# Kernel optimization log

Measured on AMD Instinct MI355X. Metric: run time of the kernel, lower is better.

## Reference

```python
import jax, jax.numpy as jnp
import numpy as np

N, P, EA, EP = 2000, 10000, 60000, 150000
F, K, L = 128, 30, 3
CUTOFF = 4.0
NUM_Z = 119  # len(ase.data.atomic_numbers)


def cosine_cutoff(d, cutoff):
    return jnp.where(d < cutoff, 0.5 * (jnp.cos(jnp.pi * d / cutoff) + 1.0), 0.0)


def sinc_expansion(d, n, cutoff):
    # d: [E,1] -> [E,n]: sin(k*pi*d/cutoff)/d, via normalized sinc
    k = jnp.arange(1, n + 1, dtype=d.dtype)
    return jnp.sinc(d * k / cutoff) * (jnp.pi * k / cutoff)


def mlp2(x, w1, b1, w2, b2):
    return jax.nn.silu(x @ w1 + b1) @ w2 + b2


def painn_update(s, v, U, V, w1, b1, w2, b2):
    Uv = jnp.einsum('nif,fg->nig', v, U)
    Vv = jnp.einsum('nif,fg->nig', v, V)
    Vv_norm = jnp.linalg.norm(Vv, axis=1)  # [n,F]
    a = mlp2(jnp.concatenate([s, Vv_norm], axis=1), w1, b1, w2, b2)  # [n,3F]
    f = s.shape[1]
    a_ss, a_sv, a_vv = a[:, :f], a[:, f:2 * f], a[:, 2 * f:]
    inner = jnp.sum(Uv * Vv, axis=1)  # [n,F]
    return s + a_ss + a_sv * inner, v + a_vv[:, None, :] * Uv


def edge_messages(sender_s, sender_v, edge_state, edge_diff, edge_dist, src,
                  fw, fb, w1, b1, w2, b2, cutoff):
    f = sender_s.shape[1]
    unit = edge_diff / jnp.maximum(jnp.linalg.norm(edge_diff, axis=1, keepdims=True), 1e-12)
    filt = (edge_state @ fw + fb) * cosine_cutoff(edge_dist, cutoff)  # [E,3F]
    out = filt * mlp2(sender_s, w1, b1, w2, b2)[src]  # gather sender scalar features
    g_sv, g_ev, g_ss = out[:, :f], out[:, f:2 * f], out[:, 2 * f:]
    msg_v = sender_v[src] * g_sv[:, None, :] + g_ev[:, None, :] * unit[:, :, None]  # [E,3,F]
    return g_ss, msg_v


def setup_inputs():
    key = jax.random.key(0)
    def nrm(i, shape, scale=0.05):
        return jax.random.normal(jax.random.fold_in(key, i), shape, dtype=jnp.float32) * scale
    atom_xyz = jax.random.uniform(jax.random.fold_in(key, 100), (N, 3), dtype=jnp.float32) * 5.0
    probe_xyz = jax.random.uniform(jax.random.fold_in(key, 101), (P, 3), dtype=jnp.float32) * 5.0
    cell = jnp.eye(3, dtype=jnp.float32) * 5.0 + nrm(102, (3, 3), 0.01)
    nodes_Z = jax.random.randint(jax.random.fold_in(key, 103), (N,), 0, NUM_Z)
    a_src = jax.random.randint(jax.random.fold_in(key, 104), (EA,), 0, N)
    a_dst = (a_src + 1 + jax.random.randint(jax.random.fold_in(key, 105), (EA,), 0, N - 1)) % N  # no self-edges
    atom_edges = jnp.stack([a_src, a_dst], axis=1)
    p_src = jax.random.randint(jax.random.fold_in(key, 106), (EP,), 0, N)
    p_dst = jax.random.randint(jax.random.fold_in(key, 107), (EP,), 0, P)
    probe_edges = jnp.stack([p_src, p_dst], axis=1)
    return dict(
        atom_xyz=atom_xyz, probe_xyz=probe_xyz, cell=cell,
        atom_edges_disp=jnp.zeros((EA, 3), jnp.float32),
        probe_edges_disp=jnp.zeros((EP, 3), jnp.float32),
        atom_embed=nrm(0, (NUM_Z, F), 1.0),
        ai_filter_w=nrm(1, (L, K, 3 * F)), ai_filter_b=nrm(2, (L, 3 * F)),
        ai_w1=nrm(3, (L, F, F)), ai_b1=nrm(4, (L, F)),
        ai_w2=nrm(5, (L, F, 3 * F)), ai_b2=nrm(6, (L, 3 * F)),
        au_U=nrm(7, (L, F, F)), au_V=nrm(8, (L, F, F)),
        au_w1=nrm(9, (L, 2 * F, F)), au_b1=nrm(10, (L, F)),
        au_w2=nrm(11, (L, F, 3 * F)), au_b2=nrm(12, (L, 3 * F)),
        pm_filter_w=nrm(13, (L, K, 3 * F)), pm_filter_b=nrm(14, (L, 3 * F)),
        pm_w1=nrm(15, (L, F, F)), pm_b1=nrm(16, (L, F)),
        pm_w2=nrm(17, (L, F, 3 * F)), pm_b2=nrm(18, (L, 3 * F)),
        pm_gw1=nrm(19, (L, F, 2 * F)), pm_gb1=nrm(20, (L, 2 * F)),
        pm_gw2=nrm(21, (L, 2 * F, 2 * F)), pm_gb2=nrm(22, (L, 2 * F)),
        pu_U=nrm(23, (L, F, F)), pu_V=nrm(24, (L, F, F)),
        pu_w1=nrm(25, (L, 2 * F, F)), pu_b1=nrm(26, (L, F)),
        pu_w2=nrm(27, (L, F, 3 * F)), pu_b2=nrm(28, (L, 3 * F)),
        nodes_Z=nodes_Z, atom_edges=atom_edges, probe_edges=probe_edges,
    )


def reference(atom_xyz, probe_xyz, cell, atom_edges_disp, probe_edges_disp, atom_embed,
              ai_filter_w, ai_filter_b, ai_w1, ai_b1, ai_w2, ai_b2,
              au_U, au_V, au_w1, au_b1, au_w2, au_b2,
              pm_filter_w, pm_filter_b, pm_w1, pm_b1, pm_w2, pm_b2,
              pm_gw1, pm_gb1, pm_gw2, pm_gb2,
              pu_U, pu_V, pu_w1, pu_b1, pu_w2, pu_b2,
              nodes_Z, atom_edges, probe_edges):
    # ---- atom representation model ----
    a_src, a_dst = atom_edges[:, 0], atom_edges[:, 1]
    a_diff = atom_xyz[a_dst] - (atom_xyz[a_src] + atom_edges_disp @ cell)  # [EA,3]
    a_dist = jnp.linalg.norm(a_diff, axis=1, keepdims=True)  # [EA,1]
    a_state = sinc_expansion(a_dist, K, CUTOFF)  # [EA,K]

    s = atom_embed[nodes_Z]  # [N,F]
    v = jnp.zeros((s.shape[0], 3, F), dtype=s.dtype)
    s_list, v_list = [], []
    for l in range(L):
        g_ss, msg_v = edge_messages(s, v, a_state, a_diff, a_dist, a_src,
                                    ai_filter_w[l], ai_filter_b[l], ai_w1[l], ai_b1[l],
                                    ai_w2[l], ai_b2[l], CUTOFF)
        s = s + jax.ops.segment_sum(g_ss, a_dst, num_segments=N)
        v = v + jax.ops.segment_sum(msg_v, a_dst, num_segments=N)
        s, v = painn_update(s, v, au_U[l], au_V[l], au_w1[l], au_b1[l], au_w2[l], au_b2[l])
        s_list.append(s)
        v_list.append(v)

    # ---- probe message model (one-way, gated update) ----
    p_src, p_dst = probe_edges[:, 0], probe_edges[:, 1]
    p_diff = probe_xyz[p_dst] - (atom_xyz[p_src] + probe_edges_disp @ cell)  # [EP,3]
    p_dist = jnp.linalg.norm(p_diff, axis=1, keepdims=True)
    p_state = sinc_expansion(p_dist, K, CUTOFF)

    ps = jnp.zeros((P, F), dtype=s.dtype)
    pv = jnp.zeros((P, 3, F), dtype=s.dtype)
    for l in range(L):
        g_ss, msg_v = edge_messages(s_list[l], v_list[l], p_state, p_diff, p_dist, p_src,
                                    pm_filter_w[l], pm_filter_b[l], pm_w1[l], pm_b1[l],
                                    pm_w2[l], pm_b2[l], CUTOFF)
        m_s = jax.ops.segment_sum(g_ss, p_dst, num_segments=P)
        m_v = jax.ops.segment_sum(msg_v, p_dst, num_segments=P)
        gate = jax.nn.sigmoid(mlp2(m_s, pm_gw1[l], pm_gb1[l], pm_gw2[l], pm_gb2[l]))  # [P,2F]
        gs, gv = gate[:, :F], gate[:, F:]
        ps = ps * gs + (1.0 - gs) * m_s
        pv = pv * gv[:, None, :] + (1.0 - gv[:, None, :]) * m_v
        ps, pv = painn_update(ps, pv, pu_U[l], pu_V[l], pu_w1[l], pu_b1[l], pu_w2[l], pu_b2[l])
    return ps, pv
```

## Files before the change

### kernel.cpp

```cpp
#include <hip/hip_runtime.h>
#include <hip/hip_bf16.h>
#include <math.h>

#define PI_F 3.14159265358979323846f

static constexpr int F = 128;
static constexpr int KB = 30;
static constexpr int LAYERS = 3;
static constexpr float CUT = 4.0f;
static constexpr int BINS = 512;

typedef short bf16x8 __attribute__((ext_vector_type(8)));
typedef float f32x4 __attribute__((ext_vector_type(4)));
typedef unsigned short u16x8 __attribute__((ext_vector_type(8)));

__device__ __forceinline__ float bf2f(unsigned short u) {
    union { unsigned int i; float f; } c; c.i = ((unsigned int)u) << 16; return c.f;
}
__device__ __forceinline__ short f2bf(float x) {
    union { float f; unsigned int u; } c; c.f = x;
    unsigned int r = c.u + 0x7FFFu + ((c.u >> 16) & 1u);
    return (short)(r >> 16);
}

__device__ __forceinline__ float edge_dist(const float* __restrict__ sxyz,
                                           const float* __restrict__ dxyz,
                                           const float* __restrict__ disp,
                                           const float* __restrict__ cell,
                                           int s, int d, int e, float* dx) {
    const float* dp = disp + 3 * (size_t)e;
#pragma unroll
    for (int i = 0; i < 3; i++) {
        float dc = dp[0] * cell[0 * 3 + i] + dp[1] * cell[1 * 3 + i] + dp[2] * cell[2 * 3 + i];
        dx[i] = dxyz[3 * d + i] - (sxyz[3 * s + i] + dc);
    }
    return sqrtf(dx[0] * dx[0] + dx[1] * dx[1] + dx[2] * dx[2]);
}

__global__ void k_count(const int* __restrict__ edges, const float* __restrict__ sxyz,
                        const float* __restrict__ dxyz, const float* __restrict__ disp,
                        const float* __restrict__ cell, int* __restrict__ cnt, int E) {
    int i = blockIdx.x * blockDim.x + threadIdx.x;
    if (i >= E) return;
    int s = edges[2 * i], d = edges[2 * i + 1];
    float dx[3];
    float dist = edge_dist(sxyz, dxyz, disp, cell, s, d, i, dx);
    if (dist < CUT) atomicAdd(&cnt[d], 1);
}

__global__ void k_scan(const int* __restrict__ cnt, int* __restrict__ off, int n) {
    __shared__ int part[1024];
    int t = threadIdx.x;
    int chunk = (n + 1023) / 1024;
    int b = t * chunk; if (b > n) b = n;
    int e = b + chunk; if (e > n) e = n;
    int s = 0;
    for (int i = b; i < e; i++) s += cnt[i];
    part[t] = s;
    __syncthreads();
    for (int o = 1; o < 1024; o <<= 1) {
        int v = part[t];
        int add = (t >= o) ? part[t - o] : 0;
        __syncthreads();
        part[t] = v + add;
        __syncthreads();
    }
    int run = (t == 0) ? 0 : part[t - 1];
    for (int i = b; i < e; i++) { off[i] = run; run += cnt[i]; }
    if (t == 1023) off[n] = part[1023];
}

__global__ void k_scatter(const int* __restrict__ edges, const float* __restrict__ sxyz,
                          const float* __restrict__ dxyz, const float* __restrict__ disp,
                          const float* __restrict__ cell, int* __restrict__ cur,
                          int* __restrict__ eids, int E) {
    int i = blockIdx.x * blockDim.x + threadIdx.x;
    if (i >= E) return;
    int s = edges[2 * i], d = edges[2 * i + 1];
    float dx[3];
    float dist = edge_dist(sxyz, dxyz, disp, cell, s, d, i, dx);
    if (dist < CUT) {
        int pos = atomicAdd(&cur[d], 1);
        eids[pos] = i;
    }
}

__global__ void k_geom_rec(const float* __restrict__ sxyz, const float* __restrict__ dxyz,
                           const float* __restrict__ disp, const float* __restrict__ cell,
                           const int* __restrict__ edges, const int* __restrict__ eids,
                           const int* __restrict__ eoff, int ndst,
                           float4* __restrict__ erec, int* __restrict__ srcs) {
    int pos = blockIdx.x * blockDim.x + threadIdx.x;
    if (pos >= eoff[ndst]) return;
    int e = eids[pos];
    int s = edges[2 * e], d = edges[2 * e + 1];
    float dx[3];
    float dist = edge_dist(sxyz, dxyz, disp, cell, s, d, e, dx);
    float inv = 1.0f / fmaxf(dist, 1e-12f);
    float db = fminf(dist * ((float)BINS / CUT), (float)BINS - 0.0001f);
    erec[pos] = make_float4(dx[0] * inv, dx[1] * inv, dx[2] * inv, db);
    srcs[pos] = s;
}

__global__ void k_sbuild(float* __restrict__ Sp) {
    int i = blockIdx.x * blockDim.x + threadIdx.x;
    if (i > BINS) return;
    float d = (float)i * (CUT / (float)BINS);
    float cc = (d < CUT) ? 0.5f * (cosf(PI_F * d / CUT) + 1.0f) : 0.0f;
    float* row = Sp + (size_t)i * 32;
#pragma unroll
    for (int k = 0; k < KB; k++) {
        float kk = (float)(k + 1);
        float st = (d > 1e-12f) ? sinf(PI_F * d * kk / CUT) / d : PI_F * kk / CUT;
        row[k] = cc * st;
    }
    row[30] = cc;
    row[31] = 0.f;
}

__global__ void k_fwpack(const float* __restrict__ ai_fw, const float* __restrict__ ai_fb,
                         const float* __restrict__ pm_fw, const float* __restrict__ pm_fb,
                         float* __restrict__ fwp) {
    int i = blockIdx.x * blockDim.x + threadIdx.x;
    if (i >= 6 * 32 * 384) return;
    int tbl = i / (32 * 384);
    int k = (i / 384) % 32;
    int c = i % 384;
    const float* fw = (tbl < 3) ? ai_fw + (size_t)tbl * KB * 384 : pm_fw + (size_t)(tbl - 3) * KB * 384;
    const float* fb = (tbl < 3) ? ai_fb + (size_t)tbl * 384 : pm_fb + (size_t)(tbl - 3) * 384;
    float v = 0.f;
    if (k < KB) v = fw[(size_t)k * 384 + c];
    else if (k == 30) v = fb[c];
    fwp[i] = v;
}

__global__ void k_tpack(const short* __restrict__ Tbf, short* __restrict__ Tp) {
    int i = blockIdx.x * blockDim.x + threadIdx.x;
    if (i >= 6 * BINS * 128) return;
    int tbl = i / (BINS * 128);
    int rem = i % (BINS * 128);
    int bin = rem >> 7, lane = rem & 127;
    const short* a = Tbf + ((size_t)tbl * (BINS + 1) + bin) * 512 + lane * 4;
    const short* b = a + 512;
    short* o = Tp + ((size_t)tbl * BINS + bin) * 1024 + lane * 8;
    o[0] = a[0]; o[1] = a[1]; o[2] = a[2]; o[3] = 0;
    o[4] = b[0]; o[5] = b[1]; o[6] = b[2]; o[7] = 0;
}

struct CvtArgs {
    const float* src[14];
    int dstoff[14];
    int Kk[14];
    int Nn[14];
};
__global__ __launch_bounds__(256) void k_cvtw(CvtArgs a, short* __restrict__ dst) {
    int arr = blockIdx.y, l = blockIdx.z;
    int K = a.Kk[arr], N = a.Nn[arr];
    int tilesx = N / 32, tilesy = K / 32;
    int tile = blockIdx.x;
    if (tile >= tilesx * tilesy) return;
    int tn = (tile % tilesx) * 32, tk = (tile / tilesx) * 32;
    __shared__ float tb[32][33];
    int tx = threadIdx.x & 31, ty = threadIdx.x >> 5;
    const float* src = a.src[arr] + (size_t)l * K * N;
    short* d = dst + a.dstoff[arr] + (size_t)l * K * N;
#pragma unroll
    for (int r = 0; r < 4; r++)
        tb[ty * 4 + r][tx] = src[(size_t)(tk + ty * 4 + r) * N + tn + tx];
    __syncthreads();
#pragma unroll
    for (int r = 0; r < 4; r++)
        d[(size_t)(tn + ty * 4 + r) * K + tk + tx] = f2bf(tb[tx][ty * 4 + r]);
}

__global__ void k_embed(const int* __restrict__ Z, const float* __restrict__ emb,
                        float* __restrict__ s, short* __restrict__ sbf, int n) {
    int i = blockIdx.x * blockDim.x + threadIdx.x;
    if (i < n * F) {
        float v = emb[(size_t)Z[i / F] * F + (i % F)];
        s[i] = v; sbf[i] = f2bf(v);
    }
}

__global__ __launch_bounds__(256) void k_gemm(const float* __restrict__ A, const float* __restrict__ B,
                                              void* __restrict__ Cout,
                                              int M, int N, int K, int outmode,
                                              int bstride, int cstride) {
    __shared__ float As[16][64];
    __shared__ float Bs[16][64];
    const float* Bz = B + (size_t)blockIdx.z * bstride;
    int tid = threadIdx.x;
    int bm = blockIdx.y * 64, bn = blockIdx.x * 64;
    int tx = tid & 15, ty = tid >> 4;
    float acc[4][4] = {};
    int arow = tid >> 2;
    int acol = (tid & 3) * 4;
    int brow = tid >> 4;
    int bcol = (tid & 15) * 4;
    for (int k0 = 0; k0 < K; k0 += 16) {
        float4 av = make_float4(0.f, 0.f, 0.f, 0.f);
        int gm = bm + arow;
        if (gm < M) av = *reinterpret_cast<const float4*>(A + (size_t)gm * K + k0 + acol);
        As[acol + 0][arow] = av.x; As[acol + 1][arow] = av.y;
        As[acol + 2][arow] = av.z; As[acol + 3][arow] = av.w;
        float4 bv = *reinterpret_cast<const float4*>(Bz + (size_t)(k0 + brow) * N + bn + bcol);
        Bs[brow][bcol + 0] = bv.x; Bs[brow][bcol + 1] = bv.y;
        Bs[brow][bcol + 2] = bv.z; Bs[brow][bcol + 3] = bv.w;
        __syncthreads();
#pragma unroll
        for (int k = 0; k < 16; k++) {
            float a0 = As[k][ty * 4 + 0], a1 = As[k][ty * 4 + 1];
            float a2 = As[k][ty * 4 + 2], a3 = As[k][ty * 4 + 3];
            float b0 = Bs[k][tx * 4 + 0], b1 = Bs[k][tx * 4 + 1];
            float b2 = Bs[k][tx * 4 + 2], b3 = Bs[k][tx * 4 + 3];
            acc[0][0] += a0 * b0; acc[0][1] += a0 * b1; acc[0][2] += a0 * b2; acc[0][3] += a0 * b3;
            acc[1][0] += a1 * b0; acc[1][1] += a1 * b1; acc[1][2] += a1 * b2; acc[1][3] += a1 * b3;
            acc[2][0] += a2 * b0; acc[2][1] += a2 * b1; acc[2][2] += a2 * b2; acc[2][3] += a2 * b3;
            acc[3][0] += a3 * b0; acc[3][1] += a3 * b1; acc[3][2] += a3 * b2; acc[3][3] += a3 * b3;
        }
        __syncthreads();
    }
#pragma unroll
    for (int i = 0; i < 4; i++) {
        int gm = bm + ty * 4 + i;
        if (gm >= M) continue;
#pragma unroll
        for (int j = 0; j < 4; j++) {
            int gn = bn + tx * 4 + j;
            float v = acc[i][j];
            if (outmode == 0) ((float*)Cout)[(size_t)gm * N + gn] = v;
            else ((short*)Cout)[(size_t)blockIdx.z * cstride + (size_t)gm * 512 + (gn & 127) * 4 + (gn >> 7)] = f2bf(v);
        }
    }
}

__device__ __forceinline__ void mfma_tile_gA(
    const short* __restrict__ A, int arows, int Astride, int row0,
    const short* __restrict__ Bt, int Bstride, int col0, int K,
    int lane, f32x4 acc[4][4]) {
    const int l15 = lane & 15, l16 = lane >> 4;
    for (int k0 = 0; k0 < K; k0 += 32) {
        const int kbase = k0 + l16 * 8;
        bf16x8 af[4], bfr[4];
#pragma unroll
        for (int i = 0; i < 4; i++) {
            int r = row0 + i * 16 + l15;
            bf16x8 t = {};
            if (r < arows) t = *reinterpret_cast<const bf16x8*>(A + (size_t)r * Astride + kbase);
            af[i] = t;
        }
#pragma unroll
        for (int j = 0; j < 4; j++)
            bfr[j] = *reinterpret_cast<const bf16x8*>(Bt + (size_t)(col0 + j * 16 + l15) * Bstride + kbase);
#pragma unroll
        for (int i = 0; i < 4; i++)
#pragma unroll
            for (int j = 0; j < 4; j++)
                acc[i][j] = __builtin_amdgcn_mfma_f32_16x16x32_bf16(af[i], bfr[j], acc[i][j], 0, 0, 0);
    }
}
__device__ __forceinline__ void mfma_tile_lA(
    const short* __restrict__ Alds, int Astride, int lrow0,
    const short* __restrict__ Bt, int Bstride, int col0, int K,
    int lane, f32x4 acc[4][4]) {
    const int l15 = lane & 15, l16 = lane >> 4;
    for (int k0 = 0; k0 < K; k0 += 32) {
        const int kbase = k0 + l16 * 8;
        bf16x8 af[4], bfr[4];
#pragma unroll
        for (int i = 0; i < 4; i++)
            af[i] = *reinterpret_cast<const bf16x8*>(Alds + (size_t)(lrow0 + i * 16 + l15) * Astride + kbase);
#pragma unroll
        for (int j = 0; j < 4; j++)
            bfr[j] = *reinterpret_cast<const bf16x8*>(Bt + (size_t)(col0 + j * 16 + l15) * Bstride + kbase);
#pragma unroll
        for (int i = 0; i < 4; i++)
#pragma unroll
            for (int j = 0; j < 4; j++)
                acc[i][j] = __builtin_amdgcn_mfma_f32_16x16x32_bf16(af[i], bfr[j], acc[i][j], 0, 0, 0);
    }
}

__global__ __launch_bounds__(512) void k_mlp2(
    const short* __restrict__ X, const short* __restrict__ w1t, const float* __restrict__ b1,
    const short* __restrict__ w2t, const float* __restrict__ b2,
    short* __restrict__ PV, int M,
    long xzs, long w1zs, long b1zs, long w2zs, long b2zs, long pvzs) {
    __shared__ short hL[64][136];
    const int z = blockIdx.z;
    const int wave = threadIdx.x >> 6, lane = threadIdx.x & 63;
    const int l15 = lane & 15, l16 = lane >> 4;
    const int rows0 = blockIdx.x * 64;
    const short* Xz = X + (size_t)z * xzs;
    if (wave < 2) {
        f32x4 acc[4][4] = {};
        mfma_tile_gA(Xz, M, 128, rows0, w1t + (size_t)z * w1zs, 128, wave * 64, 128, lane, acc);
        const float* b1z = b1 + (size_t)z * b1zs;
#pragma unroll
        for (int j = 0; j < 4; j++) {
            int cn = wave * 64 + j * 16 + l15;
            float bb = b1z[cn];
#pragma unroll
            for (int i = 0; i < 4; i++)
#pragma unroll
                for (int r = 0; r < 4; r++) {
                    float v = acc[i][j][r] + bb;
                    v = v / (1.0f + expf(-v));
                    hL[i * 16 + l16 * 4 + r][cn] = f2bf(v);
                }
        }
    }
    __syncthreads();
    if (wave < 6) {
        f32x4 acc[4][4] = {};
        mfma_tile_lA(&hL[0][0], 136, 0, w2t + (size_t)z * w2zs, 128, wave * 64, 128, lane, acc);
        const float* b2z = b2 + (size_t)z * b2zs;
        short* PVz = PV + (size_t)z * pvzs;
#pragma unroll
        for (int j = 0; j < 4; j++) {
            int gn = wave * 64 + j * 16 + l15;
            float bb = b2z[gn];
#pragma unroll
            for (int i = 0; i < 4; i++)
#pragma unroll
                for (int r = 0; r < 4; r++) {
                    int gm = rows0 + i * 16 + l16 * 4 + r;
                    if (gm < M)
                        PVz[(size_t)gm * 1024 + (gn & 127) * 8 + (gn >> 7)] = f2bf(acc[i][j][r] + bb);
                }
        }
    }
}

__global__ __launch_bounds__(512) void k_paiupd(
    const short* __restrict__ Avv,
    const float* __restrict__ s_in,
    const float* __restrict__ v_in,
    const short* __restrict__ Ut, const short* __restrict__ Vt,
    const short* __restrict__ w1t, const float* __restrict__ b1,
    const short* __restrict__ w2t, const float* __restrict__ b2,
    float* __restrict__ s_out, float* __restrict__ v_out,
    short* __restrict__ s_out_bf, short* __restrict__ v_out_pk,
    short* __restrict__ abuf, int n) {
    __shared__ short UvL[192][136];
    __shared__ short VvL[192][136];
    __shared__ short catL[64][264];
    __shared__ short hL[64][136];
    const int wave = threadIdx.x >> 6, lane = threadIdx.x & 63;
    const int l15 = lane & 15, l16 = lane >> 4;
    const int rows0 = blockIdx.x * 64;
    const int vr0 = rows0 * 3;
    if (wave < 6) {
        const int chunk = wave % 3;
        const short* Bt = (wave < 3) ? Ut : Vt;
        short (*dst)[136] = (wave < 3) ? UvL : VvL;
#pragma unroll
        for (int half = 0; half < 2; half++) {
            f32x4 acc[4][4] = {};
            mfma_tile_gA(Avv, 3 * n, 128, vr0 + chunk * 64, Bt, 128, half * 64, 128, lane, acc);
#pragma unroll
            for (int j = 0; j < 4; j++) {
                int cn = half * 64 + j * 16 + l15;
#pragma unroll
                for (int i = 0; i < 4; i++)
#pragma unroll
                    for (int r = 0; r < 4; r++)
                        dst[chunk * 64 + i * 16 + l16 * 4 + r][cn] = f2bf(acc[i][j][r]);
            }
        }
    }
    __syncthreads();
    for (int it = 0; it < 16; it++) {
        int idx = it * 512 + threadIdx.x;
        int r = idx >> 7, g = idx & 127;
        int row = rows0 + r;
        float sv = (row < n) ? s_in[(size_t)row * 128 + g] : 0.f;
        float w0 = bf2f(VvL[3 * r + 0][g]);
        float w1 = bf2f(VvL[3 * r + 1][g]);
        float w2 = bf2f(VvL[3 * r + 2][g]);
        catL[r][g] = f2bf(sv);
        catL[r][128 + g] = f2bf(sqrtf(w0 * w0 + w1 * w1 + w2 * w2));
    }
    __syncthreads();
    if (wave < 2) {
        f32x4 acc[4][4] = {};
        mfma_tile_lA(&catL[0][0], 264, 0, w1t, 256, wave * 64, 256, lane, acc);
#pragma unroll
        for (int j = 0; j < 4; j++) {
            int cn = wave * 64 + j * 16 + l15;
            float bb = b1[cn];
#pragma unroll
            for (int i = 0; i < 4; i++)
#pragma unroll
                for (int r = 0; r < 4; r++) {
                    float v = acc[i][j][r] + bb;
                    v = v / (1.0f + expf(-v));
                    hL[i * 16 + l16 * 4 + r][cn] = f2bf(v);
                }
        }
    }
    __syncthreads();
    if (wave < 6) {
        f32x4 acc[4][4] = {};
        mfma_tile_lA(&hL[0][0], 136, 0, w2t, 128, wave * 64, 128, lane, acc);
#pragma unroll
        for (int j = 0; j < 4; j++) {
            int gn = wave * 64 + j * 16 + l15;
            float bb = b2[gn];
#pragma unroll
            for (int i = 0; i < 4; i++)
#pragma unroll
                for (int r = 0; r < 4; r++) {
                    int gm = rows0 + i * 16 + l16 * 4 + r;
                    if (gm < n) abuf[(size_t)gm * 384 + gn] = f2bf(acc[i][j][r] + bb);
                }
        }
    }
    __threadfence_block();
    __syncthreads();
    for (int it = 0; it < 16; it++) {
        int idx = it * 512 + threadIdx.x;
        int r = idx >> 7, g = idx & 127;
        int row = rows0 + r;
        if (row >= n) continue;
        float u0 = bf2f(UvL[3 * r + 0][g]);
        float u1 = bf2f(UvL[3 * r + 1][g]);
        float u2 = bf2f(UvL[3 * r + 2][g]);
        float w0 = bf2f(VvL[3 * r + 0][g]);
        float w1 = bf2f(VvL[3 * r + 1][g]);
        float w2 = bf2f(VvL[3 * r + 2][g]);
        float inner = u0 * w0 + u1 * w1 + u2 * w2;
        const short* arow = abuf + (size_t)row * 384;
        float ass = bf2f(arow[g]), asv = bf2f(arow[128 + g]), avv = bf2f(arow[256 + g]);
        size_t so = (size_t)row * 128 + g;
        float snew = s_in[so] + ass + asv * inner;
        s_out[so] = snew;
        if (s_out_bf) s_out_bf[so] = f2bf(snew);
        size_t b = (size_t)row * 384;
        float r0 = v_in[b + g] + avv * u0;
        float r1 = v_in[b + 128 + g] + avv * u1;
        float r2 = v_in[b + 256 + g] + avv * u2;
        v_out[b + g] = r0;
        v_out[b + 128 + g] = r1;
        v_out[b + 256 + g] = r2;
        if (v_out_pk) {
            size_t pb = (size_t)row * 1024 + (size_t)g * 8;
            v_out_pk[pb + 4] = f2bf(r0);
            v_out_pk[pb + 5] = f2bf(r1);
            v_out_pk[pb + 6] = f2bf(r2);
        }
    }
}

__global__ __launch_bounds__(512) void k_probe_layer(
    const short* __restrict__ ms, const short* __restrict__ mv,
    const short* __restrict__ g1t, const float* __restrict__ gb1,
    const short* __restrict__ g2t, const float* __restrict__ gb2,
    const short* __restrict__ Ut, const short* __restrict__ Vt,
    const short* __restrict__ w1t, const float* __restrict__ b1,
    const short* __restrict__ w2t, const float* __restrict__ b2,
    float* __restrict__ ps, float* __restrict__ pv,
    short* __restrict__ abuf, int P, int first) {
    __shared__ short S0[192 * 136];
    __shared__ short S1[192 * 136];
    __shared__ short S2[192 * 136];
    const int tid = threadIdx.x;
    const int wave = tid >> 6, lane = tid & 63;
    const int l15 = lane & 15, l16 = lane >> 4;
    const int rows0 = blockIdx.x * 64;
    if (wave < 4) {
        f32x4 acc[4][4] = {};
        mfma_tile_gA(ms, P, 128, rows0, g1t, 128, wave * 64, 128, lane, acc);
#pragma unroll
        for (int j = 0; j < 4; j++) {
            int cn = wave * 64 + j * 16 + l15;
            float bb = gb1[cn];
#pragma unroll
            for (int i = 0; i < 4; i++)
#pragma unroll
                for (int r = 0; r < 4; r++) {
                    float v = acc[i][j][r] + bb;
                    v = v / (1.0f + expf(-v));
                    S0[(i * 16 + l16 * 4 + r) * 264 + cn] = f2bf(v);
                }
        }
    }
    __syncthreads();
    if (wave < 4) {
        f32x4 acc[4][4] = {};
        mfma_tile_lA(S0, 264, 0, g2t, 256, wave * 64, 256, lane, acc);
#pragma unroll
        for (int j = 0; j < 4; j++) {
            int cn = wave * 64 + j * 16 + l15;
            float bb = gb2[cn];
#pragma unroll
            for (int i = 0; i < 4; i++)
#pragma unroll
                for (int r = 0; r < 4; r++) {
                    float v = acc[i][j][r] + bb;
                    S1[(i * 16 + l16 * 4 + r) * 264 + cn] = f2bf(1.0f / (1.0f + expf(-v)));
                }
        }
    }
    __syncthreads();
    for (int it = 0; it < 16; it++) {
        int idx = it * 512 + tid;
        int r = idx >> 7, g = idx & 127;
        int row = rows0 + r;
        if (row < P) {
            float gs = bf2f(S1[r * 264 + g]);
            float gv = bf2f(S1[r * 264 + 128 + g]);
            size_t o = (size_t)row * 128 + g;
            float pso = first ? 0.f : ps[o];
            ps[o] = pso * gs + (1.0f - gs) * bf2f(ms[o]);
#pragma unroll
            for (int i3 = 0; i3 < 3; i3++) {
                size_t o3 = ((size_t)row * 3 + i3) * 128 + g;
                float pvo = first ? 0.f : pv[o3];
                float val = pvo * gv + (1.0f - gv) * bf2f(mv[o3]);
                pv[o3] = val;
                S2[(3 * r + i3) * 136 + g] = f2bf(val);
            }
        } else {
#pragma unroll
            for (int i3 = 0; i3 < 3; i3++) S2[(3 * r + i3) * 136 + g] = 0;
        }
    }
    __threadfence_block();
    __syncthreads();
    if (wave < 6) {
        const int chunk = wave % 3;
        const short* Bt = (wave < 3) ? Ut : Vt;
        short* dst = (wave < 3) ? S0 : S1;
#pragma unroll
        for (int half = 0; half < 2; half++) {
            f32x4 acc[4][4] = {};
            mfma_tile_lA(S2, 136, chunk * 64, Bt, 128, half * 64, 128, lane, acc);
#pragma unroll
            for (int j = 0; j < 4; j++) {
                int cn = half * 64 + j * 16 + l15;
#pragma unroll
                for (int i = 0; i < 4; i++)
#pragma unroll
                    for (int r = 0; r < 4; r++)
                        dst[(chunk * 64 + i * 16 + l16 * 4 + r) * 136 + cn] = f2bf(acc[i][j][r]);
            }
        }
    }
    __syncthreads();
    for (int it = 0; it < 16; it++) {
        int idx = it * 512 + tid;
        int r = idx >> 7, g = idx & 127;
        int row = rows0 + r;
        float sv = (row < P) ? ps[(size_t)row * 128 + g] : 0.f;
        float w0 = bf2f(S1[(3 * r + 0) * 136 + g]);
        float w1 = bf2f(S1[(3 * r + 1) * 136 + g]);
        float w2 = bf2f(S1[(3 * r + 2) * 136 + g]);
        S2[r * 264 + g] = f2bf(sv);
        S2[r * 264 + 128 + g] = f2bf(sqrtf(w0 * w0 + w1 * w1 + w2 * w2));
    }
    __syncthreads();
    if (wave < 2) {
        f32x4 acc[4][4] = {};
        mfma_tile_lA(S2, 264, 0, w1t, 256, wave * 64, 256, lane, acc);
#pragma unroll
        for (int j = 0; j < 4; j++) {
            int cn = wave * 64 + j * 16 + l15;
            float bb = b1[cn];
#pragma unroll
            for (int i = 0; i < 4; i++)
#pragma unroll
                for (int r = 0; r < 4; r++) {
                    float v = acc[i][j][r] + bb;
                    v = v / (1.0f + expf(-v));
                    S2[16896 + (i * 16 + l16 * 4 + r) * 136 + cn] = f2bf(v);
                }
        }
    }
    __syncthreads();
    if (wave < 6) {
        f32x4 acc[4][4] = {};
        mfma_tile_lA(S2 + 16896, 136, 0, w2t, 128, wave * 64, 128, lane, acc);
#pragma unroll
        for (int j = 0; j < 4; j++) {
            int gn = wave * 64 + j * 16 + l15;
            float bb = b2[gn];
#pragma unroll
            for (int i = 0; i < 4; i++)
#pragma unroll
                for (int r = 0; r < 4; r++) {
                    int gm = rows0 + i * 16 + l16 * 4 + r;
                    if (gm < P) abuf[(size_t)gm * 384 + gn] = f2bf(acc[i][j][r] + bb);
                }
        }
    }
    __threadfence_block();
    __syncthreads();
    for (int it = 0; it < 16; it++) {
        int idx = it * 512 + tid;
        int r = idx >> 7, g = idx & 127;
        int row = rows0 + r;
        if (row >= P) continue;
        float u0 = bf2f(S0[(3 * r + 0) * 136 + g]);
        float u1 = bf2f(S0[(3 * r + 1) * 136 + g]);
        float u2 = bf2f(S0[(3 * r + 2) * 136 + g]);
        float w0 = bf2f(S1[(3 * r + 0) * 136 + g]);
        float w1 = bf2f(S1[(3 * r + 1) * 136 + g]);
        float w2 = bf2f(S1[(3 * r + 2) * 136 + g]);
        float inner = u0 * w0 + u1 * w1 + u2 * w2;
        const short* arow = abuf + (size_t)row * 384;
        float ass = bf2f(arow[g]), asv = bf2f(arow[128 + g]), avv = bf2f(arow[256 + g]);
        size_t so = (size_t)row * 128 + g;
        ps[so] = ps[so] + ass + asv * inner;
        size_t b = (size_t)row * 384;
        pv[b + g] += avv * u0;
        pv[b + 128 + g] += avv * u1;
        pv[b + 256 + g] += avv * u2;
    }
}

__global__ __launch_bounds__(256) void k_gather_ns(
    const float4* __restrict__ erec, const int* __restrict__ srcs,
    const int* __restrict__ eoff, const short* __restrict__ Tp,
    const short* __restrict__ PV,
    const float* __restrict__ s_in, const float* __restrict__ v_in,
    float* __restrict__ s_out, float* __restrict__ v_out,
    short* __restrict__ s_out_bf, short* __restrict__ v_out_bf, int ndst,
    long tzs, long pvzs, long mszs, long mvzs) {
    const int t = threadIdx.x & 127;
    const int half = threadIdx.x >> 7;
    const int z = blockIdx.z;
    const short* __restrict__ T = Tp + (size_t)z * tzs;
    const short* __restrict__ PVz = PV + (size_t)z * pvzs;
    short* __restrict__ msz = s_out_bf ? s_out_bf + (size_t)z * mszs : nullptr;
    short* __restrict__ mvz = v_out_bf ? v_out_bf + (size_t)z * mvzs : nullptr;

    for (int d = blockIdx.x * 2 + half; d < ndst; d += gridDim.x * 2) {
        const int e0 = eoff[d], e1 = eoff[d + 1];
        float accs = 0.f, av0 = 0.f, av1 = 0.f, av2 = 0.f;

        auto ACC = [&](const float4& u, int bin, u16x8 Tv, u16x8 Pv) {
            const float fr = u.w - (float)bin;
            const float f0 = fmaf(fr, bf2f(Tv[4]) - bf2f(Tv[0]), bf2f(Tv[0]));
            const float f1 = fmaf(fr, bf2f(Tv[5]) - bf2f(Tv[1]), bf2f(Tv[1]));
            const float f2 = fmaf(fr, bf2f(Tv[6]) - bf2f(Tv[2]), bf2f(Tv[2]));
            const float gsv = f0 * bf2f(Pv[0]);
            const float gev = f1 * bf2f(Pv[1]);
            accs += f2 * bf2f(Pv[2]);
            av0 = fmaf(bf2f(Pv[4]), gsv, fmaf(gev, u.x, av0));
            av1 = fmaf(bf2f(Pv[5]), gsv, fmaf(gev, u.y, av1));
            av2 = fmaf(bf2f(Pv[6]), gsv, fmaf(gev, u.z, av2));
        };

        int ii = e0;
        for (; ii + 3 < e1; ii += 4) {
            const float4 u0 = erec[ii + 0], u1 = erec[ii + 1];
            const float4 u2 = erec[ii + 2], u3 = erec[ii + 3];
            const int s0 = srcs[ii + 0], s1 = srcs[ii + 1];
            const int s2 = srcs[ii + 2], s3 = srcs[ii + 3];
            const int b0 = (int)u0.w, b1 = (int)u1.w, b2 = (int)u2.w, b3 = (int)u3.w;
            const u16x8 T0 = *(const u16x8*)(T + ((size_t)b0 * 128 + t) * 8);
            const u16x8 T1 = *(const u16x8*)(T + ((size_t)b1 * 128 + t) * 8);
            const u16x8 T2 = *(const u16x8*)(T + ((size_t)b2 * 128 + t) * 8);
            const u16x8 T3 = *(const u16x8*)(T + ((size_t)b3 * 128 + t) * 8);
            const u16x8 P0 = *(const u16x8*)(PVz + ((size_t)s0 * 128 + t) * 8);
            const u16x8 P1 = *(const u16x8*)(PVz + ((size_t)s1 * 128 + t) * 8);
            const u16x8 P2 = *(const u16x8*)(PVz + ((size_t)s2 * 128 + t) * 8);
            const u16x8 P3 = *(const u16x8*)(PVz + ((size_t)s3 * 128 + t) * 8);
            ACC(u0, b0, T0, P0); ACC(u1, b1, T1, P1);
            ACC(u2, b2, T2, P2); ACC(u3, b3, T3, P3);
        }
        for (; ii < e1; ++ii) {
            const float4 u = erec[ii];
            const int s = srcs[ii];
            const int b = (int)u.w;
            const u16x8 Tv = *(const u16x8*)(T + ((size_t)b * 128 + t) * 8);
            const u16x8 Pv = *(const u16x8*)(PVz + ((size_t)s * 128 + t) * 8);
            ACC(u, b, Tv, Pv);
        }

        if (s_in) {
            accs += s_in[(size_t)d * 128 + t];
            av0 += v_in[(size_t)d * 384 + t];
            av1 += v_in[(size_t)d * 384 + 128 + t];
            av2 += v_in[(size_t)d * 384 + 256 + t];
        }
        if (s_out) {
            s_out[(size_t)d * 128 + t] = accs;
            v_out[(size_t)d * 384 + t] = av0;
            v_out[(size_t)d * 384 + 128 + t] = av1;
            v_out[(size_t)d * 384 + 256 + t] = av2;
        }
        if (msz) msz[(size_t)d * 128 + t] = f2bf(accs);
        if (mvz) {
            mvz[(size_t)(3 * d + 0) * 128 + t] = f2bf(av0);
            mvz[(size_t)(3 * d + 1) * 128 + t] = f2bf(av1);
            mvz[(size_t)(3 * d + 2) * 128 + t] = f2bf(av2);
        }
    }
}

__global__ __launch_bounds__(512) void k_gather_sp(
    const float4* __restrict__ erec, const int* __restrict__ srcs,
    const int* __restrict__ eoff, const short* __restrict__ Tp,
    const short* __restrict__ PV,
    const float* __restrict__ s_in, const float* __restrict__ v_in,
    float* __restrict__ s_out, float* __restrict__ v_out,
    short* __restrict__ s_out_bf, short* __restrict__ v_out_bf, int ndst,
    long tzs, long pvzs, long mszs, long mvzs) {
    __shared__ float red[2][128][4];
    const int tid = threadIdx.x;
    const int t = tid & 127;
    const int split = (tid >> 7) & 1;
    const int dsel = tid >> 8;
    const int z = blockIdx.z;
    const short* __restrict__ T = Tp + (size_t)z * tzs;
    const short* __restrict__ PVz = PV + (size_t)z * pvzs;
    short* __restrict__ msz = s_out_bf ? s_out_bf + (size_t)z * mszs : nullptr;
    short* __restrict__ mvz = v_out_bf ? v_out_bf + (size_t)z * mvzs : nullptr;

    const int d = blockIdx.x * 2 + dsel;
    const bool valid = d < ndst;
    int e0 = 0, e1 = 0;
    if (valid) { e0 = eoff[d]; e1 = eoff[d + 1]; }
    const int emid = e0 + ((e1 - e0 + 1) >> 1);
    const int lo = split ? emid : e0;
    const int hi = split ? e1 : emid;

    float accs = 0.f, av0 = 0.f, av1 = 0.f, av2 = 0.f;

    auto ACC = [&](const float4& u, int bin, u16x8 Tv, u16x8 Pv) {
        const float fr = u.w - (float)bin;
        const float f0 = fmaf(fr, bf2f(Tv[4]) - bf2f(Tv[0]), bf2f(Tv[0]));
        const float f1 = fmaf(fr, bf2f(Tv[5]) - bf2f(Tv[1]), bf2f(Tv[1]));
        const float f2 = fmaf(fr, bf2f(Tv[6]) - bf2f(Tv[2]), bf2f(Tv[2]));
        const float gsv = f0 * bf2f(Pv[0]);
        const float gev = f1 * bf2f(Pv[1]);
        accs += f2 * bf2f(Pv[2]);
        av0 = fmaf(bf2f(Pv[4]), gsv, fmaf(gev, u.x, av0));
        av1 = fmaf(bf2f(Pv[5]), gsv, fmaf(gev, u.y, av1));
        av2 = fmaf(bf2f(Pv[6]), gsv, fmaf(gev, u.z, av2));
    };

    int ii = lo;
    for (; ii + 3 < hi; ii += 4) {
        const float4 u0 = erec[ii + 0], u1 = erec[ii + 1];
        const float4 u2 = erec[ii + 2], u3 = erec[ii + 3];
        const int s0 = srcs[ii + 0], s1 = srcs[ii + 1];
        const int s2 = srcs[ii + 2], s3 = srcs[ii + 3];
        const int b0 = (int)u0.w, b1 = (int)u1.w, b2 = (int)u2.w, b3 = (int)u3.w;
        const u16x8 T0 = *(const u16x8*)(T + ((size_t)b0 * 128 + t) * 8);
        const u16x8 T1 = *(const u16x8*)(T + ((size_t)b1 * 128 + t) * 8);
        const u16x8 T2 = *(const u16x8*)(T + ((size_t)b2 * 128 + t) * 8);
        const u16x8 T3 = *(const u16x8*)(T + ((size_t)b3 * 128 + t) * 8);
        const u16x8 P0 = *(const u16x8*)(PVz + ((size_t)s0 * 128 + t) * 8);
        const u16x8 P1 = *(const u16x8*)(PVz + ((size_t)s1 * 128 + t) * 8);
        const u16x8 P2 = *(const u16x8*)(PVz + ((size_t)s2 * 128 + t) * 8);
        const u16x8 P3 = *(const u16x8*)(PVz + ((size_t)s3 * 128 + t) * 8);
        ACC(u0, b0, T0, P0); ACC(u1, b1, T1, P1);
        ACC(u2, b2, T2, P2); ACC(u3, b3, T3, P3);
    }
    for (; ii < hi; ++ii) {
        const float4 u = erec[ii];
        const int s = srcs[ii];
        const int b = (int)u.w;
        const u16x8 Tv = *(const u16x8*)(T + ((size_t)b * 128 + t) * 8);
        const u16x8 Pv = *(const u16x8*)(PVz + ((size_t)s * 128 + t) * 8);
        ACC(u, b, Tv, Pv);
    }

    if (split) {
        red[dsel][t][0] = accs; red[dsel][t][1] = av0;
        red[dsel][t][2] = av1;  red[dsel][t][3] = av2;
    }
    __syncthreads();
    if (!split && valid) {
        accs += red[dsel][t][0];
        av0 += red[dsel][t][1];
        av1 += red[dsel][t][2];
        av2 += red[dsel][t][3];
        if (s_in) {
            accs += s_in[(size_t)d * 128 + t];
            av0 += v_in[(size_t)d * 384 + t];
            av1 += v_in[(size_t)d * 384 + 128 + t];
            av2 += v_in[(size_t)d * 384 + 256 + t];
        }
        if (s_out) {
            s_out[(size_t)d * 128 + t] = accs;
            v_out[(size_t)d * 384 + t] = av0;
            v_out[(size_t)d * 384 + 128 + t] = av1;
            v_out[(size_t)d * 384 + 256 + t] = av2;
        }
        if (msz) msz[(size_t)d * 128 + t] = f2bf(accs);
        if (mvz) {
            mvz[(size_t)(3 * d + 0) * 128 + t] = f2bf(av0);
            mvz[(size_t)(3 * d + 1) * 128 + t] = f2bf(av1);
            mvz[(size_t)(3 * d + 2) * 128 + t] = f2bf(av2);
        }
    }
}

extern "C" void kernel_launch(void* const* d_in, const int* in_sizes, int n_in,
                              void* d_out, int out_size, void* d_ws, size_t ws_size,
                              hipStream_t stream) {
    const float* atom_xyz  = (const float*)d_in[0];
    const float* probe_xyz = (const float*)d_in[1];
    const float* cell      = (const float*)d_in[2];
    const float* a_disp    = (const float*)d_in[3];
    const float* p_disp    = (const float*)d_in[4];
    const float* atom_embed= (const float*)d_in[5];
    const float* ai_fw = (const float*)d_in[6];
    const float* ai_fb = (const float*)d_in[7];
    const float* ai_b1 = (const float*)d_in[9];
    const float* ai_b2 = (const float*)d_in[11];
    const float* au_b1 = (const float*)d_in[15];
    const float* au_b2 = (const float*)d_in[17];
    const float* pm_fw = (const float*)d_in[18];
    const float* pm_fb = (const float*)d_in[19];
    const float* pm_b1 = (const float*)d_in[21];
    const float* pm_b2 = (const float*)d_in[23];
    const float* pm_gb1= (const float*)d_in[25];
    const float* pm_gb2= (const float*)d_in[27];
    const float* pu_b1 = (const float*)d_in[31];
    const float* pu_b2 = (const float*)d_in[33];
    const int* nodes_Z = (const int*)d_in[34];
    const int* a_edges = (const int*)d_in[35];
    const int* p_edges = (const int*)d_in[36];

    const int N  = in_sizes[34];
    const int EA = in_sizes[35] / 2;
    const int EP = in_sizes[36] / 2;
    const int P  = in_sizes[1] / 3;

    enum { W_AI_W1=0, W_AI_W2, W_AU_U, W_AU_V, W_AU_W1, W_AU_W2, W_PM_W1, W_PM_W2,
           W_PM_GW1, W_PM_GW2, W_PU_U, W_PU_V, W_PU_W1, W_PU_W2 };
    const int wsrc[14] = {8,10,12,13,14,16,20,22,24,26,28,29,30,32};
    const int wK[14]   = {128,128,128,128,256,128,128,128,128,256,128,128,256,128};
    const int wN[14]   = {128,384,128,128,128,384,128,384,256,256,128,128,128,384};
    size_t woff[15]; woff[0] = 0;
    for (int i = 0; i < 14; i++) woff[i + 1] = woff[i] + (size_t)3 * wK[i] * wN[i];

    char* w = (char*)d_ws;
    size_t off = 0;
    auto alloc = [&](size_t bytes) -> void* {
        void* p = w + off;
        off = (off + bytes + 255) & ~(size_t)255;
        return p;
    };
    int* a_off  = (int*)alloc((size_t)(N + 1) * 4);
    int* a_cur  = (int*)alloc((size_t)N * 4);
    int* a_eids = (int*)alloc((size_t)EA * 4);
    int* a_srcs = (int*)alloc((size_t)EA * 4);
    int* p_off  = (int*)alloc((size_t)(P + 1) * 4);
    int* p_cur  = (int*)alloc((size_t)P * 4);
    int* p_eids = (int*)alloc((size_t)EP * 4);
    int* p_srcs = (int*)alloc((size_t)EP * 4);
    float4* a_erec = (float4*)alloc((size_t)EA * 16);
    float4* p_erec = (float4*)alloc((size_t)EP * 16);
    float* Sp   = (float*)alloc((size_t)(BINS + 1) * 32 * 4);
    float* fwp  = (float*)alloc((size_t)6 * 32 * 384 * 4);
    short* Tbf  = (short*)alloc((size_t)6 * (BINS + 1) * 512 * 2);
    short* Tp   = (short*)alloc((size_t)6 * BINS * 1024 * 2);
    short* wbt  = (short*)alloc(woff[14] * 2);
    float* s0     = (float*)alloc((size_t)N * F * 4);
    float* v0     = (float*)alloc((size_t)N * 3 * F * 4);
    float* s_list = (float*)alloc((size_t)LAYERS * N * F * 4);
    float* v_list = (float*)alloc((size_t)LAYERS * N * 3 * F * 4);
    float* msf    = (float*)alloc((size_t)N * F * 4);
    float* mvf    = (float*)alloc((size_t)N * 3 * F * 4);
    short* s0_bf    = (short*)alloc((size_t)N * F * 2);
    short* sbf_list = (short*)alloc((size_t)LAYERS * N * F * 2);
    short* vpk8     = (short*)alloc((size_t)4 * N * 1024 * 2);
    short* ms3      = (short*)alloc((size_t)3 * P * F * 2);
    short* mv3      = (short*)alloc((size_t)3 * 3 * P * F * 2);
    short* mv_bf    = (short*)alloc((size_t)N * 3 * F * 2);
    short* abuf_bf  = (short*)alloc((size_t)P * 3 * F * 2);
    (void)ws_size; (void)n_in;

    hipMemsetAsync(a_cur, 0, (size_t)N * 4, stream);
    k_count<<<(EA + 255) / 256, 256, 0, stream>>>(a_edges, atom_xyz, atom_xyz, a_disp, cell, a_cur, EA);
    k_scan<<<1, 1024, 0, stream>>>(a_cur, a_off, N);
    hipMemcpyAsync(a_cur, a_off, (size_t)N * 4, hipMemcpyDeviceToDevice, stream);
    k_scatter<<<(EA + 255) / 256, 256, 0, stream>>>(a_edges, atom_xyz, atom_xyz, a_disp, cell, a_cur, a_eids, EA);
    hipMemsetAsync(p_cur, 0, (size_t)P * 4, stream);
    k_count<<<(EP + 255) / 256, 256, 0, stream>>>(p_edges, atom_xyz, probe_xyz, p_disp, cell, p_cur, EP);
    k_scan<<<1, 1024, 0, stream>>>(p_cur, p_off, P);
    hipMemcpyAsync(p_cur, p_off, (size_t)P * 4, hipMemcpyDeviceToDevice, stream);
    k_scatter<<<(EP + 255) / 256, 256, 0, stream>>>(p_edges, atom_xyz, probe_xyz, p_disp, cell, p_cur, p_eids, EP);

    k_geom_rec<<<(EA + 255) / 256, 256, 0, stream>>>(atom_xyz, atom_xyz, a_disp, cell, a_edges,
                                                     a_eids, a_off, N, a_erec, a_srcs);
    k_geom_rec<<<(EP + 255) / 256, 256, 0, stream>>>(atom_xyz, probe_xyz, p_disp, cell, p_edges,
                                                     p_eids, p_off, P, p_erec, p_srcs);

    k_sbuild<<<(BINS + 256) / 256, 256, 0, stream>>>(Sp);
    k_fwpack<<<(6 * 32 * 384 + 255) / 256, 256, 0, stream>>>(ai_fw, ai_fb, pm_fw, pm_fb, fwp);
    {
        dim3 g(384 / 64, (BINS + 1 + 63) / 64, 6);
        k_gemm<<<g, 256, 0, stream>>>(Sp, fwp, Tbf, BINS + 1, 384, 32, 4, 32 * 384, (BINS + 1) * 512);
    }
    k_tpack<<<(6 * BINS * 128 + 255) / 256, 256, 0, stream>>>(Tbf, Tp);

    {
        CvtArgs ca;
        for (int i = 0; i < 14; i++) {
            ca.src[i] = (const float*)d_in[wsrc[i]];
            ca.dstoff[i] = (int)woff[i];
            ca.Kk[i] = wK[i]; ca.Nn[i] = wN[i];
        }
        k_cvtw<<<dim3(64, 14, 3), 256, 0, stream>>>(ca, wbt);
    }
    auto wt = [&](int a, int l) { return wbt + woff[a] + (size_t)l * wK[a] * wN[a]; };

    k_embed<<<(N * F + 255) / 256, 256, 0, stream>>>(nodes_Z, atom_embed, s0, s0_bf, N);
    hipMemsetAsync(v0, 0, (size_t)N * 3 * F * 4, stream);
    hipMemsetAsync(vpk8, 0, (size_t)N * 1024 * 2, stream);

    auto pvbuf = [&](int idx) { return vpk8 + (size_t)idx * N * 1024; };
    const int nb_atom = (N + 63) / 64;
    const int nb_probe = (P + 63) / 64;

    for (int l = 0; l < LAYERS; l++) {
        const float* scur = l ? (s_list + (size_t)(l - 1) * N * F) : s0;
        const float* vcur = l ? (v_list + (size_t)(l - 1) * N * 3 * F) : v0;
        const short* scur_bf = l ? (sbf_list + (size_t)(l - 1) * N * F) : s0_bf;
        k_mlp2<<<dim3(nb_atom, 1, 1), 512, 0, stream>>>(
            scur_bf, wt(W_AI_W1, l), ai_b1 + (size_t)l * F,
            wt(W_AI_W2, l), ai_b2 + (size_t)l * 3 * F,
            pvbuf(l), N, 0, 0, 0, 0, 0, 0);
        k_gather_sp<<<dim3((N + 1) / 2, 1, 1), 512, 0, stream>>>(a_erec, a_srcs, a_off,
                 Tp + (size_t)l * BINS * 1024, pvbuf(l),
                 scur, vcur, msf, mvf, nullptr, mv_bf, N, 0, 0, 0, 0);
        k_paiupd<<<dim3(nb_atom), 512, 0, stream>>>(
            mv_bf, msf, mvf,
            wt(W_AU_U, l), wt(W_AU_V, l),
            wt(W_AU_W1, l), au_b1 + (size_t)l * F,
            wt(W_AU_W2, l), au_b2 + (size_t)l * 3 * F,
            s_list + (size_t)l * N * F, v_list + (size_t)l * N * 3 * F,
            sbf_list + (size_t)l * N * F, pvbuf(l + 1), abuf_bf, N);
    }

    float* ps = (float*)d_out;
    float* pv = (float*)d_out + (size_t)P * F;

    k_mlp2<<<dim3(nb_atom, 1, 3), 512, 0, stream>>>(
        sbf_list, wt(W_PM_W1, 0), pm_b1, wt(W_PM_W2, 0), pm_b2,
        pvbuf(1), N,
        (long)N * F, (long)128 * 128, 128, (long)128 * 384, 384, (long)N * 1024);

    k_gather_ns<<<dim3((P + 1) / 2, 1, 3), 256, 0, stream>>>(p_erec, p_srcs, p_off,
             Tp + (size_t)3 * BINS * 1024, pvbuf(1),
             nullptr, nullptr, nullptr, nullptr, ms3, mv3, P,
             (long)BINS * 1024, (long)N * 1024, (long)P * F, (long)3 * P * F);

    for (int l = 0; l < LAYERS; l++) {
        k_probe_layer<<<dim3(nb_probe), 512, 0, stream>>>(
            ms3 + (size_t)l * P * F, mv3 + (size_t)l * 3 * P * F,
            wt(W_PM_GW1, l), pm_gb1 + (size_t)l * 2 * F,
            wt(W_PM_GW2, l), pm_gb2 + (size_t)l * 2 * F,
            wt(W_PU_U, l), wt(W_PU_V, l),
            wt(W_PU_W1, l), pu_b1 + (size_t)l * F,
            wt(W_PU_W2, l), pu_b2 + (size_t)l * 3 * F,
            ps, pv, abuf_bf, P, l == 0);
    }
}
```

Before: 706.2 us.

## Pack gather tables to 6 bf16 per lane and rebalance MFMA work across waves

Drops the two padding slots from the packed per-lane filter table and sender-feature rows, going from 8 to 6 bf16 values. Gathers now issue 12-byte loads instead of 16-byte ones, which cuts the bytes fetched per edge in the memory-bound gather kernels. Separately, the MLP and PaiNN-update GEMM stages are retiled so all 8 waves of each block do MFMA work, instead of only 2, 4 or 6 while the rest idle. The 12-byte loads are only 4-byte aligned and may split into several load instructions, and the smaller per-wave tiles reuse each B fragment less.

```diff
diff --git a/kernel.cpp b/kernel.cpp
--- a/kernel.cpp
+++ b/kernel.cpp
@@ -9,13 +9,21 @@
 static constexpr int LAYERS = 3;
 static constexpr float CUT = 4.0f;
 static constexpr int BINS = 512;
+static constexpr int ROWW = 768;
 
 typedef short bf16x8 __attribute__((ext_vector_type(8)));
 typedef float f32x4 __attribute__((ext_vector_type(4)));
-typedef unsigned short u16x8 __attribute__((ext_vector_type(8)));
+
+struct __attribute__((packed, aligned(4))) U6 { unsigned int w0, w1, w2; };
 
 __device__ __forceinline__ float bf2f(unsigned short u) {
     union { unsigned int i; float f; } c; c.i = ((unsigned int)u) << 16; return c.f;
+}
+__device__ __forceinline__ float blo(unsigned int w) {
+    union { unsigned int i; float f; } c; c.i = w << 16; return c.f;
+}
+__device__ __forceinline__ float bhi(unsigned int w) {
+    union { unsigned int i; float f; } c; c.i = w & 0xffff0000u; return c.f;
 }
 __device__ __forceinline__ short f2bf(float x) {
     union { float f; unsigned int u; } c; c.f = x;
@@ -142,9 +150,9 @@
     int bin = rem >> 7, lane = rem & 127;
     const short* a = Tbf + ((size_t)tbl * (BINS + 1) + bin) * 512 + lane * 4;
     const short* b = a + 512;
-    short* o = Tp + ((size_t)tbl * BINS + bin) * 1024 + lane * 8;
-    o[0] = a[0]; o[1] = a[1]; o[2] = a[2]; o[3] = 0;
-    o[4] = b[0]; o[5] = b[1]; o[6] = b[2]; o[7] = 0;
+    short* o = Tp + ((size_t)tbl * BINS + bin) * ROWW + lane * 6;
+    o[0] = a[0]; o[1] = a[1]; o[2] = a[2];
+    o[3] = b[0]; o[4] = b[1]; o[5] = b[2];
 }
 
 struct CvtArgs {
@@ -234,16 +242,17 @@
     }
 }
 
-__device__ __forceinline__ void mfma_tile_gA(
+template<int RF>
+__device__ __forceinline__ void mfma_g(
     const short* __restrict__ A, int arows, int Astride, int row0,
     const short* __restrict__ Bt, int Bstride, int col0, int K,
-    int lane, f32x4 acc[4][4]) {
+    int lane, f32x4 acc[RF][4]) {
     const int l15 = lane & 15, l16 = lane >> 4;
     for (int k0 = 0; k0 < K; k0 += 32) {
         const int kbase = k0 + l16 * 8;
-        bf16x8 af[4], bfr[4];
-#pragma unroll
-        for (int i = 0; i < 4; i++) {
+        bf16x8 af[RF], bfr[4];
+#pragma unroll
+        for (int i = 0; i < RF; i++) {
             int r = row0 + i * 16 + l15;
             bf16x8 t = {};
             if (r < arows) t = *reinterpret_cast<const bf16x8*>(A + (size_t)r * Astride + kbase);
@@ -253,28 +262,29 @@
         for (int j = 0; j < 4; j++)
             bfr[j] = *reinterpret_cast<const bf16x8*>(Bt + (size_t)(col0 + j * 16 + l15) * Bstride + kbase);
 #pragma unroll
-        for (int i = 0; i < 4; i++)
+        for (int i = 0; i < RF; i++)
 #pragma unroll
             for (int j = 0; j < 4; j++)
                 acc[i][j] = __builtin_amdgcn_mfma_f32_16x16x32_bf16(af[i], bfr[j], acc[i][j], 0, 0, 0);
     }
 }
-__device__ __forceinline__ void mfma_tile_lA(
+template<int RF>
+__device__ __forceinline__ void mfma_l(
     const short* __restrict__ Alds, int Astride, int lrow0,
     const short* __restrict__ Bt, int Bstride, int col0, int K,
-    int lane, f32x4 acc[4][4]) {
+    int lane, f32x4 acc[RF][4]) {
     const int l15 = lane & 15, l16 = lane >> 4;
     for (int k0 = 0; k0 < K; k0 += 32) {
         const int kbase = k0 + l16 * 8;
-        bf16x8 af[4], bfr[4];
-#pragma unroll
-        for (int i = 0; i < 4; i++)
+        bf16x8 af[RF], bfr[4];
+#pragma unroll
+        for (int i = 0; i < RF; i++)
             af[i] = *reinterpret_cast<const bf16x8*>(Alds + (size_t)(lrow0 + i * 16 + l15) * Astride + kbase);
 #pragma unroll
         for (int j = 0; j < 4; j++)
             bfr[j] = *reinterpret_cast<const bf16x8*>(Bt + (size_t)(col0 + j * 16 + l15) * Bstride + kbase);
 #pragma unroll
-        for (int i = 0; i < 4; i++)
+        for (int i = 0; i < RF; i++)
 #pragma unroll
             for (int j = 0; j < 4; j++)
                 acc[i][j] = __builtin_amdgcn_mfma_f32_16x16x32_bf16(af[i], bfr[j], acc[i][j], 0, 0, 0);
@@ -292,41 +302,41 @@
     const int l15 = lane & 15, l16 = lane >> 4;
     const int rows0 = blockIdx.x * 64;
     const short* Xz = X + (size_t)z * xzs;
-    if (wave < 2) {
-        f32x4 acc[4][4] = {};
-        mfma_tile_gA(Xz, M, 128, rows0, w1t + (size_t)z * w1zs, 128, wave * 64, 128, lane, acc);
+    {
+        const int rowblk = wave & 3, colh = wave >> 2;
+        f32x4 acc[1][4] = {};
+        mfma_g<1>(Xz, M, 128, rows0 + rowblk * 16, w1t + (size_t)z * w1zs, 128, colh * 64, 128, lane, acc);
         const float* b1z = b1 + (size_t)z * b1zs;
 #pragma unroll
         for (int j = 0; j < 4; j++) {
-            int cn = wave * 64 + j * 16 + l15;
+            int cn = colh * 64 + j * 16 + l15;
             float bb = b1z[cn];
 #pragma unroll
-            for (int i = 0; i < 4; i++)
+            for (int r = 0; r < 4; r++) {
+                float v = acc[0][j][r] + bb;
+                v = v / (1.0f + expf(-v));
+                hL[rowblk * 16 + l16 * 4 + r][cn] = f2bf(v);
+            }
+        }
+    }
+    __syncthreads();
+    short* PVz = PV + (size_t)z * pvzs;
+    const float* b2z = b2 + (size_t)z * b2zs;
+    for (int task = wave; task < 12; task += 8) {
+        const int rowh = task & 1, colb = task >> 1;
+        f32x4 acc[2][4] = {};
+        mfma_l<2>(&hL[0][0], 136, rowh * 32, w2t + (size_t)z * w2zs, 128, colb * 64, 128, lane, acc);
+#pragma unroll
+        for (int j = 0; j < 4; j++) {
+            int gn = colb * 64 + j * 16 + l15;
+            float bb = b2z[gn];
+#pragma unroll
+            for (int i = 0; i < 2; i++)
 #pragma unroll
                 for (int r = 0; r < 4; r++) {
-                    float v = acc[i][j][r] + bb;
-                    v = v / (1.0f + expf(-v));
-                    hL[i * 16 + l16 * 4 + r][cn] = f2bf(v);
-                }
-        }
-    }
-    __syncthreads();
-    if (wave < 6) {
-        f32x4 acc[4][4] = {};
-        mfma_tile_lA(&hL[0][0], 136, 0, w2t + (size_t)z * w2zs, 128, wave * 64, 128, lane, acc);
-        const float* b2z = b2 + (size_t)z * b2zs;
-        short* PVz = PV + (size_t)z * pvzs;
-#pragma unroll
-        for (int j = 0; j < 4; j++) {
-            int gn = wave * 64 + j * 16 + l15;
-            float bb = b2z[gn];
-#pragma unroll
-            for (int i = 0; i < 4; i++)
-#pragma unroll
-                for (int r = 0; r < 4; r++) {
-                    int gm = rows0 + i * 16 + l16 * 4 + r;
+                    int gm = rows0 + rowh * 32 + i * 16 + l16 * 4 + r;
                     if (gm < M)
-                        PVz[(size_t)gm * 1024 + (gn & 127) * 8 + (gn >> 7)] = f2bf(acc[i][j][r] + bb);
+                        PVz[(size_t)gm * ROWW + (gn & 127) * 6 + (gn >> 7)] = f2bf(acc[i][j][r] + bb);
                 }
         }
     }
@@ -350,23 +360,21 @@
     const int l15 = lane & 15, l16 = lane >> 4;
     const int rows0 = blockIdx.x * 64;
     const int vr0 = rows0 * 3;
-    if (wave < 6) {
-        const int chunk = wave % 3;
-        const short* Bt = (wave < 3) ? Ut : Vt;
-        short (*dst)[136] = (wave < 3) ? UvL : VvL;
-#pragma unroll
-        for (int half = 0; half < 2; half++) {
-            f32x4 acc[4][4] = {};
-            mfma_tile_gA(Avv, 3 * n, 128, vr0 + chunk * 64, Bt, 128, half * 64, 128, lane, acc);
-#pragma unroll
-            for (int j = 0; j < 4; j++) {
-                int cn = half * 64 + j * 16 + l15;
-#pragma unroll
-                for (int i = 0; i < 4; i++)
-#pragma unroll
-                    for (int r = 0; r < 4; r++)
-                        dst[chunk * 64 + i * 16 + l16 * 4 + r][cn] = f2bf(acc[i][j][r]);
-            }
+    for (int task = wave; task < 12; task += 8) {
+        const int uv = task >= 6;
+        const int rem = task - uv * 6;
+        const int chunk = rem >> 1, half = rem & 1;
+        f32x4 acc[4][4] = {};
+        mfma_g<4>(Avv, 3 * n, 128, vr0 + chunk * 64, uv ? Vt : Ut, 128, half * 64, 128, lane, acc);
+        short (*dst)[136] = uv ? VvL : UvL;
+#pragma unroll
+        for (int j = 0; j < 4; j++) {
+            int cn = half * 64 + j * 16 + l15;
+#pragma unroll
+            for (int i = 0; i < 4; i++)
+#pragma unroll
+                for (int r = 0; r < 4; r++)
+                    dst[chunk * 64 + i * 16 + l16 * 4 + r][cn] = f2bf(acc[i][j][r]);
         }
     }
     __syncthreads();
@@ -382,36 +390,36 @@
         catL[r][128 + g] = f2bf(sqrtf(w0 * w0 + w1 * w1 + w2 * w2));
     }
     __syncthreads();
-    if (wave < 2) {
-        f32x4 acc[4][4] = {};
-        mfma_tile_lA(&catL[0][0], 264, 0, w1t, 256, wave * 64, 256, lane, acc);
-#pragma unroll
-        for (int j = 0; j < 4; j++) {
-            int cn = wave * 64 + j * 16 + l15;
+    {
+        const int rowblk = wave & 3, colh = wave >> 2;
+        f32x4 acc[1][4] = {};
+        mfma_l<1>(&catL[0][0], 264, rowblk * 16, w1t, 256, colh * 64, 256, lane, acc);
+#pragma unroll
+        for (int j = 0; j < 4; j++) {
+            int cn = colh * 64 + j * 16 + l15;
             float bb = b1[cn];
 #pragma unroll
-            for (int i = 0; i < 4; i++)
+            for (int r = 0; r < 4; r++) {
+                float v = acc[0][j][r] + bb;
+                v = v / (1.0f + expf(-v));
+                hL[rowblk * 16 + l16 * 4 + r][cn] = f2bf(v);
+            }
+        }
+    }
+    __syncthreads();
+    for (int task = wave; task < 12; task += 8) {
+        const int rowh = task & 1, colb = task >> 1;
+        f32x4 acc[2][4] = {};
+        mfma_l<2>(&hL[0][0], 136, rowh * 32, w2t, 128, colb * 64, 128, lane, acc);
+#pragma unroll
+        for (int j = 0; j < 4; j++) {
+            int gn = colb * 64 + j * 16 + l15;
+            float bb = b2[gn];
+#pragma unroll
+            for (int i = 0; i < 2; i++)
 #pragma unroll
                 for (int r = 0; r < 4; r++) {
-                    float v = acc[i][j][r] + bb;
-                    v = v / (1.0f + expf(-v));
-                    hL[i * 16 + l16 * 4 + r][cn] = f2bf(v);
-                }
-        }
-    }
-    __syncthreads();
-    if (wave < 6) {
-        f32x4 acc[4][4] = {};
-        mfma_tile_lA(&hL[0][0], 136, 0, w2t, 128, wave * 64, 128, lane, acc);
-#pragma unroll
-        for (int j = 0; j < 4; j++) {
-            int gn = wave * 64 + j * 16 + l15;
-            float bb = b2[gn];
-#pragma unroll
-            for (int i = 0; i < 4; i++)
-#pragma unroll
-                for (int r = 0; r < 4; r++) {
-                    int gm = rows0 + i * 16 + l16 * 4 + r;
+                    int gm = rows0 + rowh * 32 + i * 16 + l16 * 4 + r;
                     if (gm < n) abuf[(size_t)gm * 384 + gn] = f2bf(acc[i][j][r] + bb);
                 }
         }
@@ -444,10 +452,10 @@
         v_out[b + 128 + g] = r1;
         v_out[b + 256 + g] = r2;
         if (v_out_pk) {
-            size_t pb = (size_t)row * 1024 + (size_t)g * 8;
-            v_out_pk[pb + 4] = f2bf(r0);
-            v_out_pk[pb + 5] = f2bf(r1);
-            v_out_pk[pb + 6] = f2bf(r2);
+            size_t pb = (size_t)row * ROWW + (size_t)g * 6;
+            v_out_pk[pb + 3] = f2bf(r0);
+            v_out_pk[pb + 4] = f2bf(r1);
+            v_out_pk[pb + 5] = f2bf(r2);
         }
     }
 }
@@ -468,37 +476,39 @@
     const int wave = tid >> 6, lane = tid & 63;
     const int l15 = lane & 15, l16 = lane >> 4;
     const int rows0 = blockIdx.x * 64;
-    if (wave < 4) {
-        f32x4 acc[4][4] = {};
-        mfma_tile_gA(ms, P, 128, rows0, g1t, 128, wave * 64, 128, lane, acc);
-#pragma unroll
-        for (int j = 0; j < 4; j++) {
-            int cn = wave * 64 + j * 16 + l15;
+    {
+        const int rowh = wave >> 2, colq = wave & 3;
+        f32x4 acc[2][4] = {};
+        mfma_g<2>(ms, P, 128, rows0 + rowh * 32, g1t, 128, colq * 64, 128, lane, acc);
+#pragma unroll
+        for (int j = 0; j < 4; j++) {
+            int cn = colq * 64 + j * 16 + l15;
             float bb = gb1[cn];
 #pragma unroll
-            for (int i = 0; i < 4; i++)
+            for (int i = 0; i < 2; i++)
 #pragma unroll
                 for (int r = 0; r < 4; r++) {
                     float v = acc[i][j][r] + bb;
                     v = v / (1.0f + expf(-v));
-                    S0[(i * 16 + l16 * 4 + r) * 264 + cn] = f2bf(v);
+                    S0[(rowh * 32 + i * 16 + l16 * 4 + r) * 264 + cn] = f2bf(v);
                 }
         }
     }
     __syncthreads();
-    if (wave < 4) {
-        f32x4 acc[4][4] = {};
-        mfma_tile_lA(S0, 264, 0, g2t, 256, wave * 64, 256, lane, acc);
-#pragma unroll
-        for (int j = 0; j < 4; j++) {
-            int cn = wave * 64 + j * 16 + l15;
+    {
+        const int rowh = wave >> 2, colq = wave & 3;
+        f32x4 acc[2][4] = {};
+        mfma_l<2>(S0, 264, rowh * 32, g2t, 256, colq * 64, 256, lane, acc);
+#pragma unroll
+        for (int j = 0; j < 4; j++) {
+            int cn = colq * 64 + j * 16 + l15;
             float bb = gb2[cn];
 #pragma unroll
-            for (int i = 0; i < 4; i++)
+            for (int i = 0; i < 2; i++)
 #pragma unroll
                 for (int r = 0; r < 4; r++) {
                     float v = acc[i][j][r] + bb;
-                    S1[(i * 16 + l16 * 4 + r) * 264 + cn] = f2bf(1.0f / (1.0f + expf(-v)));
+                    S1[(rowh * 32 + i * 16 + l16 * 4 + r) * 264 + cn] = f2bf(1.0f / (1.0f + expf(-v)));
                 }
         }
     }
@@ -528,23 +538,21 @@
     }
     __threadfence_block();
     __syncthreads();
-    if (wave < 6) {
-        const int chunk = wave % 3;
-        const short* Bt = (wave < 3) ? Ut : Vt;
-        short* dst = (wave < 3) ? S0 : S1;
-#pragma unroll
-        for (int half = 0; half < 2; half++) {
-            f32x4 acc[4][4] = {};
-            mfma_tile_lA(S2, 136, chunk * 64, Bt, 128, half * 64, 128, lane, acc);
-#pragma unroll
-            for (int j = 0; j < 4; j++) {
-                int cn = half * 64 + j * 16 + l15;
-#pragma unroll
-                for (int i = 0; i < 4; i++)
-#pragma unroll
-                    for (int r = 0; r < 4; r++)
-                        dst[(chunk * 64 + i * 16 + l16 * 4 + r) * 136 + cn] = f2bf(acc[i][j][r]);
-            }
+    for (int task = wave; task < 12; task += 8) {
+        const int uv = task >= 6;
+        const int rem = task - uv * 6;
+        const int chunk = rem >> 1, half = rem & 1;
+        f32x4 acc[4][4] = {};
+        mfma_l<4>(S2, 136, chunk * 64, uv ? Vt : Ut, 128, half * 64, 128, lane, acc);
+        short* dst = uv ? S1 : S0;
+#pragma unroll
+        for (int j = 0; j < 4; j++) {
+            int cn = half * 64 + j * 16 + l15;
+#pragma unroll
+            for (int i = 0; i < 4; i++)
+#pragma unroll
+                for (int r = 0; r < 4; r++)
+                    dst[(chunk * 64 + i * 16 + l16 * 4 + r) * 136 + cn] = f2bf(acc[i][j][r]);
         }
     }
     __syncthreads();
@@ -560,36 +568,36 @@
         S2[r * 264 + 128 + g] = f2bf(sqrtf(w0 * w0 + w1 * w1 + w2 * w2));
     }
     __syncthreads();
-    if (wave < 2) {
-        f32x4 acc[4][4] = {};
-        mfma_tile_lA(S2, 264, 0, w1t, 256, wave * 64, 256, lane, acc);
-#pragma unroll
-        for (int j = 0; j < 4; j++) {
-            int cn = wave * 64 + j * 16 + l15;
+    {
+        const int rowblk = wave & 3, colh = wave >> 2;
+        f32x4 acc[1][4] = {};
+        mfma_l<1>(S2, 264, rowblk * 16, w1t, 256, colh * 64, 256, lane, acc);
+#pragma unroll
+        for (int j = 0; j < 4; j++) {
+            int cn = colh * 64 + j * 16 + l15;
             float bb = b1[cn];
 #pragma unroll
-            for (int i = 0; i < 4; i++)
+            for (int r = 0; r < 4; r++) {
+                float v = acc[0][j][r] + bb;
+                v = v / (1.0f + expf(-v));
+                S2[16896 + (rowblk * 16 + l16 * 4 + r) * 136 + cn] = f2bf(v);
+            }
+        }
+    }
+    __syncthreads();
+    for (int task = wave; task < 12; task += 8) {
+        const int rowh = task & 1, colb = task >> 1;
+        f32x4 acc[2][4] = {};
+        mfma_l<2>(S2 + 16896, 136, rowh * 32, w2t, 128, colb * 64, 128, lane, acc);
+#pragma unroll
+        for (int j = 0; j < 4; j++) {
+            int gn = colb * 64 + j * 16 + l15;
+            float bb = b2[gn];
+#pragma unroll
+            for (int i = 0; i < 2; i++)
 #pragma unroll
                 for (int r = 0; r < 4; r++) {
-                    float v = acc[i][j][r] + bb;
-                    v = v / (1.0f + expf(-v));
-                    S2[16896 + (i * 16 + l16 * 4 + r) * 136 + cn] = f2bf(v);
-                }
-        }
-    }
-    __syncthreads();
-    if (wave < 6) {
-        f32x4 acc[4][4] = {};
-        mfma_tile_lA(S2 + 16896, 136, 0, w2t, 128, wave * 64, 128, lane, acc);
-#pragma unroll
-        for (int j = 0; j < 4; j++) {
-            int gn = wave * 64 + j * 16 + l15;
-            float bb = b2[gn];
-#pragma unroll
-            for (int i = 0; i < 4; i++)
-#pragma unroll
-                for (int r = 0; r < 4; r++) {
-                    int gm = rows0 + i * 16 + l16 * 4 + r;
+                    int gm = rows0 + rowh * 32 + i * 16 + l16 * 4 + r;
                     if (gm < P) abuf[(size_t)gm * 384 + gn] = f2bf(acc[i][j][r] + bb);
                 }
         }
@@ -619,6 +627,21 @@
     }
 }
 
+#define GATHER_ACC(u, Tq, Pq)                                              \
+    {                                                                      \
+        const float fr = (u).w - (float)((int)(u).w);                      \
+        const float a0 = blo((Tq).w0), a1 = bhi((Tq).w0), a2 = blo((Tq).w1); \
+        const float f0 = fmaf(fr, bhi((Tq).w1) - a0, a0);                  \
+        const float f1 = fmaf(fr, blo((Tq).w2) - a1, a1);                  \
+        const float f2 = fmaf(fr, bhi((Tq).w2) - a2, a2);                  \
+        const float gsv = f0 * blo((Pq).w0);                               \
+        const float gev = f1 * bhi((Pq).w0);                               \
+        accs += f2 * blo((Pq).w1);                                         \
+        av0 = fmaf(bhi((Pq).w1), gsv, fmaf(gev, (u).x, av0));              \
+        av1 = fmaf(blo((Pq).w2), gsv, fmaf(gev, (u).y, av1));              \
+        av2 = fmaf(bhi((Pq).w2), gsv, fmaf(gev, (u).z, av2));              \
+    }
+
 __global__ __launch_bounds__(256) void k_gather_ns(
     const float4* __restrict__ erec, const int* __restrict__ srcs,
     const int* __restrict__ eoff, const short* __restrict__ Tp,
@@ -639,44 +662,29 @@
         const int e0 = eoff[d], e1 = eoff[d + 1];
         float accs = 0.f, av0 = 0.f, av1 = 0.f, av2 = 0.f;
 
-        auto ACC = [&](const float4& u, int bin, u16x8 Tv, u16x8 Pv) {
-            const float fr = u.w - (float)bin;
-            const float f0 = fmaf(fr, bf2f(Tv[4]) - bf2f(Tv[0]), bf2f(Tv[0]));
-            const float f1 = fmaf(fr, bf2f(Tv[5]) - bf2f(Tv[1]), bf2f(Tv[1]));
-            const float f2 = fmaf(fr, bf2f(Tv[6]) - bf2f(Tv[2]), bf2f(Tv[2]));
-            const float gsv = f0 * bf2f(Pv[0]);
-            const float gev = f1 * bf2f(Pv[1]);
-            accs += f2 * bf2f(Pv[2]);
-            av0 = fmaf(bf2f(Pv[4]), gsv, fmaf(gev, u.x, av0));
-            av1 = fmaf(bf2f(Pv[5]), gsv, fmaf(gev, u.y, av1));
-            av2 = fmaf(bf2f(Pv[6]), gsv, fmaf(gev, u.z, av2));
-        };
-
         int ii = e0;
         for (; ii + 3 < e1; ii += 4) {
             const float4 u0 = erec[ii + 0], u1 = erec[ii + 1];
             const float4 u2 = erec[ii + 2], u3 = erec[ii + 3];
             const int s0 = srcs[ii + 0], s1 = srcs[ii + 1];
             const int s2 = srcs[ii + 2], s3 = srcs[ii + 3];
-            const int b0 = (int)u0.w, b1 = (int)u1.w, b2 = (int)u2.w, b3 = (int)u3.w;
-            const u16x8 T0 = *(const u16x8*)(T + ((size_t)b0 * 128 + t) * 8);
-            const u16x8 T1 = *(const u16x8*)(T + ((size_t)b1 * 128 + t) * 8);
-            const u16x8 T2 = *(const u16x8*)(T + ((size_t)b2 * 128 + t) * 8);
-            const u16x8 T3 = *(const u16x8*)(T + ((size_t)b3 * 128 + t) * 8);
-            const u16x8 P0 = *(const u16x8*)(PVz + ((size_t)s0 * 128 + t) * 8);
-            const u16x8 P1 = *(const u16x8*)(PVz + ((size_t)s1 * 128 + t) * 8);
-            const u16x8 P2 = *(const u16x8*)(PVz + ((size_t)s2 * 128 + t) * 8);
-            const u16x8 P3 = *(const u16x8*)(PVz + ((size_t)s3 * 128 + t) * 8);
-            ACC(u0, b0, T0, P0); ACC(u1, b1, T1, P1);
-            ACC(u2, b2, T2, P2); ACC(u3, b3, T3, P3);
+            const U6 T0 = *(const U6*)(T + ((size_t)(int)u0.w * 128 + t) * 6);
+            const U6 T1 = *(const U6*)(T + ((size_t)(int)u1.w * 128 + t) * 6);
+            const U6 T2 = *(const U6*)(T + ((size_t)(int)u2.w * 128 + t) * 6);
+            const U6 T3 = *(const U6*)(T + ((size_t)(int)u3.w * 128 + t) * 6);
+            const U6 P0 = *(const U6*)(PVz + ((size_t)s0 * 128 + t) * 6);
+            const U6 P1 = *(const U6*)(PVz + ((size_t)s1 * 128 + t) * 6);
+            const U6 P2 = *(const U6*)(PVz + ((size_t)s2 * 128 + t) * 6);
+            const U6 P3 = *(const U6*)(PVz + ((size_t)s3 * 128 + t) * 6);
+            GATHER_ACC(u0, T0, P0); GATHER_ACC(u1, T1, P1);
+            GATHER_ACC(u2, T2, P2); GATHER_ACC(u3, T3, P3);
         }
         for (; ii < e1; ++ii) {
             const float4 u = erec[ii];
             const int s = srcs[ii];
-            const int b = (int)u.w;
-            const u16x8 Tv = *(const u16x8*)(T + ((size_t)b * 128 + t) * 8);
-            const u16x8 Pv = *(const u16x8*)(PVz + ((size_t)s * 128 + t) * 8);
-            ACC(u, b, Tv, Pv);
+            const U6 Tq = *(const U6*)(T + ((size_t)(int)u.w * 128 + t) * 6);
+            const U6 Pq = *(const U6*)(PVz + ((size_t)s * 128 + t) * 6);
+            GATHER_ACC(u, Tq, Pq);
         }
 
         if (s_in) {
@@ -729,44 +737,29 @@
 
     float accs = 0.f, av0 = 0.f, av1 = 0.f, av2 = 0.f;
 
-    auto ACC = [&](const float4& u, int bin, u16x8 Tv, u16x8 Pv) {
-        const float fr = u.w - (float)bin;
-        const float f0 = fmaf(fr, bf2f(Tv[4]) - bf2f(Tv[0]), bf2f(Tv[0]));
-        const float f1 = fmaf(fr, bf2f(Tv[5]) - bf2f(Tv[1]), bf2f(Tv[1]));
-        const float f2 = fmaf(fr, bf2f(Tv[6]) - bf2f(Tv[2]), bf2f(Tv[2]));
-        const float gsv = f0 * bf2f(Pv[0]);
-        const float gev = f1 * bf2f(Pv[1]);
-        accs += f2 * bf2f(Pv[2]);
-        av0 = fmaf(bf2f(Pv[4]), gsv, fmaf(gev, u.x, av0));
-        av1 = fmaf(bf2f(Pv[5]), gsv, fmaf(gev, u.y, av1));
-        av2 = fmaf(bf2f(Pv[6]), gsv, fmaf(gev, u.z, av2));
-    };
-
     int ii = lo;
     for (; ii + 3 < hi; ii += 4) {
         const float4 u0 = erec[ii + 0], u1 = erec[ii + 1];
         const float4 u2 = erec[ii + 2], u3 = erec[ii + 3];
         const int s0 = srcs[ii + 0], s1 = srcs[ii + 1];
         const int s2 = srcs[ii + 2], s3 = srcs[ii + 3];
-        const int b0 = (int)u0.w, b1 = (int)u1.w, b2 = (int)u2.w, b3 = (int)u3.w;
-        const u16x8 T0 = *(const u16x8*)(T + ((size_t)b0 * 128 + t) * 8);
-        const u16x8 T1 = *(const u16x8*)(T + ((size_t)b1 * 128 + t) * 8);
-        const u16x8 T2 = *(const u16x8*)(T + ((size_t)b2 * 128 + t) * 8);
-        const u16x8 T3 = *(const u16x8*)(T + ((size_t)b3 * 128 + t) * 8);
-        const u16x8 P0 = *(const u16x8*)(PVz + ((size_t)s0 * 128 + t) * 8);
-        const u16x8 P1 = *(const u16x8*)(PVz + ((size_t)s1 * 128 + t) * 8);
-        const u16x8 P2 = *(const u16x8*)(PVz + ((size_t)s2 * 128 + t) * 8);
-        const u16x8 P3 = *(const u16x8*)(PVz + ((size_t)s3 * 128 + t) * 8);
-        ACC(u0, b0, T0, P0); ACC(u1, b1, T1, P1);
-        ACC(u2, b2, T2, P2); ACC(u3, b3, T3, P3);
+        const U6 T0 = *(const U6*)(T + ((size_t)(int)u0.w * 128 + t) * 6);
+        const U6 T1 = *(const U6*)(T + ((size_t)(int)u1.w * 128 + t) * 6);
+        const U6 T2 = *(const U6*)(T + ((size_t)(int)u2.w * 128 + t) * 6);
+        const U6 T3 = *(const U6*)(T + ((size_t)(int)u3.w * 128 + t) * 6);
+        const U6 P0 = *(const U6*)(PVz + ((size_t)s0 * 128 + t) * 6);
+        const U6 P1 = *(const U6*)(PVz + ((size_t)s1 * 128 + t) * 6);
+        const U6 P2 = *(const U6*)(PVz + ((size_t)s2 * 128 + t) * 6);
+        const U6 P3 = *(const U6*)(PVz + ((size_t)s3 * 128 + t) * 6);
+        GATHER_ACC(u0, T0, P0); GATHER_ACC(u1, T1, P1);
+        GATHER_ACC(u2, T2, P2); GATHER_ACC(u3, T3, P3);
     }
     for (; ii < hi; ++ii) {
         const float4 u = erec[ii];
         const int s = srcs[ii];
-        const int b = (int)u.w;
-        const u16x8 Tv = *(const u16x8*)(T + ((size_t)b * 128 + t) * 8);
-        const u16x8 Pv = *(const u16x8*)(PVz + ((size_t)s * 128 + t) * 8);
-        ACC(u, b, Tv, Pv);
+        const U6 Tq = *(const U6*)(T + ((size_t)(int)u.w * 128 + t) * 6);
+        const U6 Pq = *(const U6*)(PVz + ((size_t)s * 128 + t) * 6);
+        GATHER_ACC(u, Tq, Pq);
     }
 
     if (split) {
@@ -860,7 +853,7 @@
     float* Sp   = (float*)alloc((size_t)(BINS + 1) * 32 * 4);
     float* fwp  = (float*)alloc((size_t)6 * 32 * 384 * 4);
     short* Tbf  = (short*)alloc((size_t)6 * (BINS + 1) * 512 * 2);
-    short* Tp   = (short*)alloc((size_t)6 * BINS * 1024 * 2);
+    short* Tp   = (short*)alloc((size_t)6 * BINS * ROWW * 2);
     short* wbt  = (short*)alloc(woff[14] * 2);
     float* s0     = (float*)alloc((size_t)N * F * 4);
     float* v0     = (float*)alloc((size_t)N * 3 * F * 4);
@@ -870,7 +863,7 @@
     float* mvf    = (float*)alloc((size_t)N * 3 * F * 4);
     short* s0_bf    = (short*)alloc((size_t)N * F * 2);
     short* sbf_list = (short*)alloc((size_t)LAYERS * N * F * 2);
-    short* vpk8     = (short*)alloc((size_t)4 * N * 1024 * 2);
+    short* vpk6     = (short*)alloc((size_t)4 * N * ROWW * 2);
     short* ms3      = (short*)alloc((size_t)3 * P * F * 2);
     short* mv3      = (short*)alloc((size_t)3 * 3 * P * F * 2);
     short* mv_bf    = (short*)alloc((size_t)N * 3 * F * 2);
@@ -914,9 +907,9 @@
 
     k_embed<<<(N * F + 255) / 256, 256, 0, stream>>>(nodes_Z, atom_embed, s0, s0_bf, N);
     hipMemsetAsync(v0, 0, (size_t)N * 3 * F * 4, stream);
-    hipMemsetAsync(vpk8, 0, (size_t)N * 1024 * 2, stream);
-
-    auto pvbuf = [&](int idx) { return vpk8 + (size_t)idx * N * 1024; };
+    hipMemsetAsync(vpk6, 0, (size_t)N * ROWW * 2, stream);
+
+    auto pvbuf = [&](int idx) { return vpk6 + (size_t)idx * N * ROWW; };
     const int nb_atom = (N + 63) / 64;
     const int nb_probe = (P + 63) / 64;
 
@@ -929,7 +922,7 @@
             wt(W_AI_W2, l), ai_b2 + (size_t)l * 3 * F,
             pvbuf(l), N, 0, 0, 0, 0, 0, 0);
         k_gather_sp<<<dim3((N + 1) / 2, 1, 1), 512, 0, stream>>>(a_erec, a_srcs, a_off,
-                 Tp + (size_t)l * BINS * 1024, pvbuf(l),
+                 Tp + (size_t)l * BINS * ROWW, pvbuf(l),
                  scur, vcur, msf, mvf, nullptr, mv_bf, N, 0, 0, 0, 0);
         k_paiupd<<<dim3(nb_atom), 512, 0, stream>>>(
             mv_bf, msf, mvf,
@@ -946,12 +939,12 @@
     k_mlp2<<<dim3(nb_atom, 1, 3), 512, 0, stream>>>(
         sbf_list, wt(W_PM_W1, 0), pm_b1, wt(W_PM_W2, 0), pm_b2,
         pvbuf(1), N,
-        (long)N * F, (long)128 * 128, 128, (long)128 * 384, 384, (long)N * 1024);
+        (long)N * F, (long)128 * 128, 128, (long)128 * 384, 384, (long)N * ROWW);
 
     k_gather_ns<<<dim3((P + 1) / 2, 1, 3), 256, 0, stream>>>(p_erec, p_srcs, p_off,
-             Tp + (size_t)3 * BINS * 1024, pvbuf(1),
+             Tp + (size_t)3 * BINS * ROWW, pvbuf(1),
              nullptr, nullptr, nullptr, nullptr, ms3, mv3, P,
-             (long)BINS * 1024, (long)N * 1024, (long)P * F, (long)3 * P * F);
+             (long)BINS * ROWW, (long)N * ROWW, (long)P * F, (long)3 * P * F);
 
     for (int l = 0; l < LAYERS; l++) {
         k_probe_layer<<<dim3(nb_probe), 512, 0, stream>>>(
```

After: 738.9 us. 4.6% more time.
